# Kernel optimization log

Measured on AMD Instinct MI355X. Metric: run time of the kernel, lower is better.

## Reference

```python
import jax, jax.numpy as jnp
import numpy as np

D = 1024
H = 16
HD = D // H
FF = 4096
B = 2
S = 2048


def _layer_norm(x, g, b, eps=1e-5):
    mu = jnp.mean(x, axis=-1, keepdims=True)
    var = jnp.mean(jnp.square(x - mu), axis=-1, keepdims=True)
    return (x - mu) * jax.lax.rsqrt(var + eps) * g + b


def setup_inputs() -> dict:
    key = jax.random.key(0)
    ks = jax.random.split(key, 16)
    s = 0.02
    return {
        "x": jax.random.normal(ks[0], (B, S, D), jnp.float32),
        "Wq": jax.random.normal(ks[1], (H, D, HD), jnp.float32) * s,
        "bq": jnp.zeros((H, HD), jnp.float32),
        "Wk": jax.random.normal(ks[2], (H, D, HD), jnp.float32) * s,
        "bk": jnp.zeros((H, HD), jnp.float32),
        "Wv": jax.random.normal(ks[3], (H, D, HD), jnp.float32) * s,
        "bv": jnp.zeros((H, HD), jnp.float32),
        "Wo": jax.random.normal(ks[4], (D, D), jnp.float32) * s,
        "bo": jnp.zeros((D,), jnp.float32),
        "W1": jax.random.normal(ks[5], (D, FF), jnp.float32) * s,
        "b1": jnp.zeros((FF,), jnp.float32),
        "W2": jax.random.normal(ks[6], (FF, D), jnp.float32) * s,
        "b2": jnp.zeros((D,), jnp.float32),
        "g1": jnp.ones((D,), jnp.float32),
        "be1": jnp.zeros((D,), jnp.float32),
        "g2": jnp.ones((D,), jnp.float32),
        "be2": jnp.zeros((D,), jnp.float32),
    }


def reference(x, Wq, bq, Wk, bk, Wv, bv, Wo, bo, W1, b1, W2, b2, g1, be1, g2, be2):
    b, s, d = x.shape
    # per-head projections (vectorized over heads)
    q = jnp.einsum("bsd,hde->bhse", x, Wq) + bq[None, :, None, :]
    k = jnp.einsum("bsd,hde->bhse", x, Wk) + bk[None, :, None, :]
    v = jnp.einsum("bsd,hde->bhse", x, Wv) + bv[None, :, None, :]
    # NOTE: source scales by 1/dim_k (not 1/sqrt(dim_k)) -- kept faithful
    scores = jnp.einsum("bhse,bhte->bhst", q, k) / jnp.asarray(HD, x.dtype)
    causal = jnp.tril(jnp.ones((s, s), bool))  # [S,S]
    scores = jnp.where(causal[None, None], scores, jnp.asarray(-jnp.inf, x.dtype))
    attn = jax.nn.softmax(scores, axis=-1)
    ctx = jnp.einsum("bhst,bhte->bhse", attn, v)  # [B,H,S,hd]
    ctx = jnp.transpose(ctx, (0, 2, 1, 3)).reshape(b, s, d)  # concat heads
    attn_out = ctx @ Wo + bo
    x = _layer_norm(x + attn_out, g1, be1)
    # feed-forward: linear -> exact GELU -> linear (dropout = eval identity)
    h = jax.nn.gelu(x @ W1 + b1, approximate=False)
    ff = h @ W2 + b2
    return _layer_norm(x + ff, g2, be2)
```

## Files before the change

kernel.cpp:

```cpp
#include <hip/hip_runtime.h>
#include <math.h>

constexpr int Dm  = 1024;
constexpr int Hh  = 16;
constexpr int HDm = 64;
constexpr int FFm = 4096;
constexpr int Bb  = 2;
constexpr int Sq  = 2048;
constexpr int Mm  = Bb * Sq;

typedef __attribute__((ext_vector_type(8))) short short8;
typedef __attribute__((ext_vector_type(4))) short short4v;
typedef __attribute__((ext_vector_type(4))) float f32x4;

#define AS1 __attribute__((address_space(1)))
#define AS3 __attribute__((address_space(3)))

constexpr float QSCALE = 0.022542110013890054f;

__device__ __forceinline__ unsigned short f2b(float f) {
    union { float f; unsigned u; } v; v.f = f;
    unsigned r = v.u + 0x7FFFu + ((v.u >> 16) & 1u);
    return (unsigned short)(r >> 16);
}

__global__ __launch_bounds__(256) void convert_x(const float* __restrict__ x,
                                                 short* __restrict__ xb) {
    int i = blockIdx.x * 256 + threadIdx.x;
    float4 v = ((const float4*)x)[i];
    short4v o;
    o[0] = (short)f2b(v.x); o[1] = (short)f2b(v.y);
    o[2] = (short)f2b(v.z); o[3] = (short)f2b(v.w);
    ((short4v*)xb)[i] = o;
}

__global__ __launch_bounds__(256) void transpose_to_bf16(
    const float* __restrict__ src, short* __restrict__ dst, int R, int C) {
    __shared__ float t[64][65];
    const int c0 = blockIdx.x * 64, r0 = blockIdx.y * 64;
    const int lc = threadIdx.x & 63, lr4 = threadIdx.x >> 6;
    #pragma unroll
    for (int p = 0; p < 16; ++p) {
        int rr = p * 4 + lr4;
        t[rr][lc] = src[(size_t)(r0 + rr) * C + c0 + lc];
    }
    __syncthreads();
    #pragma unroll
    for (int p = 0; p < 16; ++p) {
        int rr = p * 4 + lr4;
        dst[(size_t)(c0 + rr) * R + r0 + lc] = (short)f2b(t[lc][rr]);
    }
}

__global__ __launch_bounds__(256) void build_wqkv(
    const float* __restrict__ Wq, const float* __restrict__ Wk,
    const float* __restrict__ Wv, short* __restrict__ dst) {
    const int kt = blockIdx.x, h = blockIdx.y, which = blockIdx.z;
    const float* W = ((which == 0) ? Wq : (which == 1) ? Wk : Wv) +
                     (size_t)h * Dm * HDm;
    __shared__ float t[64][65];
    const int lc = threadIdx.x & 63, lr4 = threadIdx.x >> 6;
    #pragma unroll
    for (int p = 0; p < 16; ++p) {
        int kr = p * 4 + lr4;
        t[kr][lc] = W[(size_t)(kt * 64 + kr) * HDm + lc];
    }
    __syncthreads();
    const int nbase = which * 1024 + h * 64;
    #pragma unroll
    for (int p = 0; p < 16; ++p) {
        int e = p * 4 + lr4;
        dst[(size_t)(nbase + e) * Dm + kt * 64 + lc] = (short)f2b(t[lc][e]);
    }
}

__global__ __launch_bounds__(256) void build_bqkv(
    const float* __restrict__ bq, const float* __restrict__ bk,
    const float* __restrict__ bv, float* __restrict__ bcat) {
    int n = blockIdx.x * 256 + threadIdx.x;
    const float* s = (n < 1024) ? bq : (n < 2048) ? bk : bv;
    bcat[n] = s[n & 1023];
}

template<int EPI>
__global__ __launch_bounds__(512, 2) void gemm256(
    const short* __restrict__ A, const short* __restrict__ Bt,
    const float* __restrict__ bias,
    short* __restrict__ outb,
    short* __restrict__ qo, short* __restrict__ ko, short* __restrict__ vo,
    int K, int N, int NMT)
{
    __shared__ __align__(16) char lds[131072];
    char* const ldsA = lds;
    char* const ldsB = lds + 65536;
    const int tid = threadIdx.x;
    const int l = tid & 63, wv = tid >> 6;
    const int wm = wv >> 2, wn = wv & 3;
    const int lr = l & 15, lg = l >> 4;
    const int bid = blockIdx.x;
    const int m0 = (bid % NMT) * 256;
    const int n0 = (bid / NMT) * 256;
    const size_t KB = (size_t)K * 2;
    const int NT = K >> 6;

    const char* pA[2][2];
    const char* pB[2][2];
    #pragma unroll
    for (int i = 0; i < 2; ++i) {
        int c = tid + 512 * i;
        int rh = c >> 3, j = c & 7;
        int sw = (j ^ (rh & 7)) << 4;
        #pragma unroll
        for (int h = 0; h < 2; ++h) {
            pA[h][i] = (const char*)A + (size_t)(m0 + h * 128 + rh) * KB + sw;
            pB[h][i] = (const char*)Bt + (size_t)(n0 + h * 128 + rh) * KB + sw;
        }
    }
    const int dbase = tid * 16;

    f32x4 acc[8][4];
    f32x4 z4 = {0.f, 0.f, 0.f, 0.f};
    #pragma unroll
    for (int i = 0; i < 8; ++i)
        #pragma unroll
        for (int j = 0; j < 4; ++j) acc[i][j] = z4;

#define STAGE_B(h, nb) do {                                                     \
    char* _b = ldsB + ((nb) * 2 + (h)) * 16384;                                 \
    __builtin_amdgcn_global_load_lds((const AS1 void*)pB[h][0],                 \
        (AS3 void*)(_b + dbase), 16, 0, 0);                                     \
    __builtin_amdgcn_global_load_lds((const AS1 void*)pB[h][1],                 \
        (AS3 void*)(_b + dbase + 8192), 16, 0, 0);                              \
    pB[h][0] += 128; pB[h][1] += 128; } while (0)
#define STAGE_A(h, nb) do {                                                     \
    char* _a = ldsA + ((nb) * 2 + (h)) * 16384;                                 \
    __builtin_amdgcn_global_load_lds((const AS1 void*)pA[h][0],                 \
        (AS3 void*)(_a + dbase), 16, 0, 0);                                     \
    __builtin_amdgcn_global_load_lds((const AS1 void*)pA[h][1],                 \
        (AS3 void*)(_a + dbase + 8192), 16, 0, 0);                              \
    pA[h][0] += 128; pA[h][1] += 128; } while (0)

    STAGE_B(0, 0); STAGE_B(1, 0); STAGE_A(0, 0); STAGE_A(1, 0);
    asm volatile("s_waitcnt vmcnt(2)" ::: "memory");
    __builtin_amdgcn_s_barrier();
    __builtin_amdgcn_sched_barrier(0);

    const int swk0 = ((0 + lg) ^ (lr & 7)) << 4;
    const int swk1 = ((4 + lg) ^ (lr & 7)) << 4;

    for (int kt = 0; kt < NT; ++kt) {
        const int buf = kt & 1, nbuf = buf ^ 1;
        const bool more = (kt + 1 < NT);
        char* const Ah0 = ldsA + (buf * 2) * 16384;
        char* const Ah1 = ldsA + (buf * 2 + 1) * 16384;
        char* const Bh  = ldsB + (buf * 2 + (wn >> 1)) * 16384 + (wn & 1) * 8192;

        short8 bf[4][2];
        #pragma unroll
        for (int nf = 0; nf < 4; ++nf) {
            const char* bb = Bh + (nf * 16 + lr) * 128;
            bf[nf][0] = *(const short8*)(bb + swk0);
            bf[nf][1] = *(const short8*)(bb + swk1);
        }
        short8 af[2][2];

#define LOAD_A(p) do {                                                          \
    _Pragma("unroll")                                                           \
    for (int j2 = 0; j2 < 2; ++j2) {                                            \
        const int mf = 2 * (p) + j2;                                            \
        const char* ab = ((mf >> 2) ? Ah1 : Ah0) +                              \
                         ((mf & 3) * 32 + wm * 16 + lr) * 128;                  \
        af[j2][0] = *(const short8*)(ab + swk0);                                \
        af[j2][1] = *(const short8*)(ab + swk1);                                \
    } } while (0)

#define MFMA8(p) do {                                                           \
    _Pragma("unroll")                                                           \
    for (int j2 = 0; j2 < 2; ++j2)                                              \
        _Pragma("unroll")                                                       \
        for (int nf = 0; nf < 4; ++nf) {                                        \
            acc[2 * (p) + j2][nf] = __builtin_amdgcn_mfma_f32_16x16x32_bf16(    \
                af[j2][0], bf[nf][0], acc[2 * (p) + j2][nf], 0, 0, 0);          \
            acc[2 * (p) + j2][nf] = __builtin_amdgcn_mfma_f32_16x16x32_bf16(    \
                af[j2][1], bf[nf][1], acc[2 * (p) + j2][nf], 0, 0, 0);          \
        } } while (0)

        LOAD_A(0);
        if (more) STAGE_B(0, nbuf);
        __builtin_amdgcn_s_barrier();
        asm volatile("s_waitcnt lgkmcnt(0)" ::: "memory");
        __builtin_amdgcn_sched_barrier(0);
        __builtin_amdgcn_s_setprio(1);
        MFMA8(0);
        __builtin_amdgcn_s_setprio(0);
        __builtin_amdgcn_s_barrier();
        LOAD_A(1);
        if (more) STAGE_B(1, nbuf);
        __builtin_amdgcn_s_barrier();
        asm volatile("s_waitcnt lgkmcnt(0)" ::: "memory");
        __builtin_amdgcn_sched_barrier(0);
        __builtin_amdgcn_s_setprio(1);
        MFMA8(1);
        __builtin_amdgcn_s_setprio(0);
        if (more) asm volatile("s_waitcnt vmcnt(4)" ::: "memory");
        else      asm volatile("s_waitcnt vmcnt(0)" ::: "memory");
        __builtin_amdgcn_s_barrier();
        __builtin_amdgcn_sched_barrier(0);
        LOAD_A(2);
        if (more) STAGE_A(0, nbuf);
        __builtin_amdgcn_s_barrier();
        asm volatile("s_waitcnt lgkmcnt(0)" ::: "memory");
        __builtin_amdgcn_sched_barrier(0);
        __builtin_amdgcn_s_setprio(1);
        MFMA8(2);
        __builtin_amdgcn_s_setprio(0);
        __builtin_amdgcn_s_barrier();
        LOAD_A(3);
        if (more) STAGE_A(1, nbuf);
        __builtin_amdgcn_s_barrier();
        asm volatile("s_waitcnt lgkmcnt(0)" ::: "memory");
        __builtin_amdgcn_sched_barrier(0);
        __builtin_amdgcn_s_setprio(1);
        MFMA8(3);
        __builtin_amdgcn_s_setprio(0);
        asm volatile("s_waitcnt vmcnt(2)" ::: "memory");
        __builtin_amdgcn_s_barrier();
        __builtin_amdgcn_sched_barrier(0);
#undef LOAD_A
#undef MFMA8
    }

    #pragma unroll
    for (int mf = 0; mf < 8; ++mf) {
        #pragma unroll
        for (int nf = 0; nf < 4; ++nf) {
            const int n = n0 + wn * 64 + nf * 16 + lr;
            const int mB = m0 + mf * 32 + wm * 16 + lg * 4;
            if (EPI == 1) {
                #pragma unroll
                for (int r = 0; r < 4; ++r) {
                    float val = acc[mf][nf][r] + bias[n];
                    val = 0.5f * val * (1.0f + erff(val * 0.70710678118654752f));
                    outb[(size_t)(mB + r) * N + n] = (short)f2b(val);
                }
            } else {
                const int which = n >> 10, hh = (n >> 6) & 15, e = n & 63;
                const int bb2 = mB >> 11, ss = mB & 2047;
                if (which == 2) {
                    short4v pk;
                    #pragma unroll
                    for (int r = 0; r < 4; ++r)
                        pk[r] = (short)f2b(acc[mf][nf][r] + bias[n]);
                    *(short4v*)&vo[(((size_t)bb2 * Hh + hh) * HDm + e) * Sq + ss] = pk;
                } else {
                    short* o = (which == 0) ? qo : ko;
                    const float sc = (which == 0) ? QSCALE : 1.0f;
                    #pragma unroll
                    for (int r = 0; r < 4; ++r) {
                        float val = (acc[mf][nf][r] + bias[n]) * sc;
                        o[(((size_t)bb2 * Hh + hh) * Sq + ss + r) * HDm + e] = (short)f2b(val);
                    }
                }
            }
        }
    }
#undef STAGE_A
#undef STAGE_B
}

template<int EPI, int BM>
__global__ __launch_bounds__(256) void gemm_bf16(
    const short* __restrict__ A, const short* __restrict__ Bt,
    const float* __restrict__ bias, const float* __restrict__ res,
    float* __restrict__ outf, short* __restrict__ outb,
    int K, int N)
{
    constexpr int BMW = BM / 2;
    constexpr int MF  = BMW / 16;
    __shared__ __align__(16) char smem[BM * 128 + 16384];
    char* ldsA = smem;
    char* ldsB = smem + BM * 128;
    const int tid = threadIdx.x;
    const int l = tid & 63, wv = tid >> 6;
    const int wr = wv >> 1, wc = wv & 1, lr = l & 15, lg = l >> 4;
    const int m0 = blockIdx.x * BM, n0 = blockIdx.y * 128;
    const size_t KB = (size_t)K * 2;
    const char* Ab = (const char*)A;
    const char* Bb = (const char*)Bt;

    f32x4 zero4 = {0.f, 0.f, 0.f, 0.f};
    f32x4 acc[MF][4];
    #pragma unroll
    for (int i = 0; i < MF; ++i)
        #pragma unroll
        for (int j = 0; j < 4; ++j) acc[i][j] = zero4;

    for (int k0 = 0; k0 < K; k0 += 64) {
        __syncthreads();
        #pragma unroll
        for (int r = 0; r < BM / 32; ++r) {
            int c  = (wv * (BM / 32) + r) * 64;
            int cl = c + l;
            int row = cl >> 3, j = cl & 7;
            int sw = ((j ^ (row & 7)) << 4);
            __builtin_amdgcn_global_load_lds(
                (const AS1 void*)(Ab + (size_t)(m0 + row) * KB + (size_t)k0 * 2 + sw),
                (AS3 void*)(ldsA + c * 16), 16, 0, 0);
        }
        #pragma unroll
        for (int r = 0; r < 4; ++r) {
            int c  = (wv * 4 + r) * 64;
            int cl = c + l;
            int row = cl >> 3, j = cl & 7;
            int sw = ((j ^ (row & 7)) << 4);
            __builtin_amdgcn_global_load_lds(
                (const AS1 void*)(Bb + (size_t)(n0 + row) * KB + (size_t)k0 * 2 + sw),
                (AS3 void*)(ldsB + c * 16), 16, 0, 0);
        }
        __syncthreads();
        #pragma unroll
        for (int ks = 0; ks < 2; ++ks) {
            short8 af[MF], bf[4];
            #pragma unroll
            for (int i = 0; i < MF; ++i) {
                int rowA = wr * BMW + i * 16 + lr;
                af[i] = *(const short8*)(ldsA + rowA * 128 +
                            (((ks * 4 + lg) ^ (rowA & 7)) << 4));
            }
            #pragma unroll
            for (int i = 0; i < 4; ++i) {
                int rowB = wc * 64 + i * 16 + lr;
                bf[i] = *(const short8*)(ldsB + rowB * 128 +
                            (((ks * 4 + lg) ^ (rowB & 7)) << 4));
            }
            #pragma unroll
            for (int i = 0; i < MF; ++i)
                #pragma unroll
                for (int jn = 0; jn < 4; ++jn)
                    acc[i][jn] = __builtin_amdgcn_mfma_f32_16x16x32_bf16(
                        af[i], bf[jn], acc[i][jn], 0, 0, 0);
        }
    }

    #pragma unroll
    for (int i = 0; i < MF; ++i) {
        #pragma unroll
        for (int jn = 0; jn < 4; ++jn) {
            #pragma unroll
            for (int r = 0; r < 4; ++r) {
                int m = m0 + wr * BMW + i * 16 + lg * 4 + r;
                int n = n0 + wc * 64 + jn * 16 + lr;
                float val = acc[i][jn][r];
                if (EPI == 0) {
                    val += bias[n] + res[(size_t)m * N + n];
                    outf[(size_t)m * N + n] = val;
                } else {
                    val += bias[n];
                    val = 0.5f * val * (1.0f + erff(val * 0.70710678118654752f));
                    outb[(size_t)m * N + n] = (short)f2b(val);
                }
            }
        }
    }
}

__global__ __launch_bounds__(256) void attn_mfma(
    const short* __restrict__ qg, const short* __restrict__ kg,
    const short* __restrict__ vtg, short* __restrict__ ctx)
{
    const int bid = blockIdx.x;
    const int qt = (Sq / 64 - 1) - (bid >> 5);
    const int hb = bid & 31;
    const int h = hb & 15, b = hb >> 4;
    const int tid = threadIdx.x;
    const int l = tid & 63, wv = tid >> 6;
    const int lr = l & 15, lg = l >> 4;

    __shared__ __align__(16) char KlB[8192];
    __shared__ __align__(16) char VtB[8192];
    __shared__ __align__(16) char PlB[4][2048];

    const size_t bh = ((size_t)b * Hh + h) * Sq;
    const size_t vbase = ((size_t)b * Hh + h) * HDm * Sq;

    const int qbase = qt * 64 + wv * 16;
    short8 aq[2];
    #pragma unroll
    for (int ks = 0; ks < 2; ++ks)
        aq[ks] = *(const short8*)(qg + (bh + qbase + lr) * HDm + ks * 32 + lg * 8);

    f32x4 zero4 = {0.f, 0.f, 0.f, 0.f};
    f32x4 oacc[4], lacc = zero4;
    #pragma unroll
    for (int i = 0; i < 4; ++i) oacc[i] = zero4;
    float mreg[4];
    #pragma unroll
    for (int r = 0; r < 4; ++r) mreg[r] = -3e38f;

    short8 vone;
    #pragma unroll
    for (int j = 0; j < 8; ++j) vone[j] = (short)0x3F80;

    char* plw = PlB[wv];

    const char* srcK[2]; const char* srcV[2];
    #pragma unroll
    for (int r2 = 0; r2 < 2; ++r2) {
        int cl = tid + 256 * r2;
        int row = cl >> 3, j = cl & 7;
        srcK[r2] = (const char*)kg + ((bh + row) * HDm + ((j ^ (row & 7)) * 8)) * 2;
        srcV[r2] = (const char*)vtg + (vbase + (size_t)row * Sq + ((j ^ (row & 7)) * 8)) * 2;
    }

    const int nt = qt + 1;
    for (int tk = 0; tk < nt; ++tk) {
        __syncthreads();
        #pragma unroll
        for (int r2 = 0; r2 < 2; ++r2) {
            int c = tid + 256 * r2;
            __builtin_amdgcn_global_load_lds((const AS1 void*)srcK[r2],
                (AS3 void*)(KlB + c * 16), 16, 0, 0);
            srcK[r2] += 64 * HDm * 2;
            __builtin_amdgcn_global_load_lds((const AS1 void*)srcV[r2],
                (AS3 void*)(VtB + c * 16), 16, 0, 0);
            srcV[r2] += 64 * 2;
        }
        __syncthreads();

        f32x4 sc[4];
        #pragma unroll
        for (int i = 0; i < 4; ++i) sc[i] = zero4;
        __builtin_amdgcn_s_setprio(1);
        #pragma unroll
        for (int kd = 0; kd < 2; ++kd) {
            #pragma unroll
            for (int nf = 0; nf < 4; ++nf) {
                short8 bk = *(const short8*)(KlB + (nf * 16 + lr) * 128 +
                                (((kd * 4 + lg) ^ (lr & 7)) << 4));
                sc[nf] = __builtin_amdgcn_mfma_f32_16x16x32_bf16(
                    aq[kd], bk, sc[nf], 0, 0, 0);
            }
        }
        __builtin_amdgcn_s_setprio(0);

        if (tk == qt) {
            #pragma unroll
            for (int r = 0; r < 4; ++r) {
                const int qglob = qbase + lg * 4 + r;
                #pragma unroll
                for (int nf = 0; nf < 4; ++nf)
                    if (tk * 64 + nf * 16 + lr > qglob) sc[nf][r] = -3e38f;
            }
        }

        float lm[4];
        #pragma unroll
        for (int r = 0; r < 4; ++r)
            lm[r] = fmaxf(fmaxf(sc[0][r], sc[1][r]), fmaxf(sc[2][r], sc[3][r]));
        bool grow = (lm[0] > mreg[0] + 8.f) || (lm[1] > mreg[1] + 8.f) ||
                    (lm[2] > mreg[2] + 8.f) || (lm[3] > mreg[3] + 8.f);

        if (__any((int)grow)) {
            #pragma unroll
            for (int r = 0; r < 4; ++r) {
                float mr = lm[r];
                #pragma unroll
                for (int o = 1; o < 16; o <<= 1)
                    mr = fmaxf(mr, __shfl_xor(mr, o));
                float mnew = fmaxf(mreg[r], mr);
                float cf = exp2f(mreg[r] - mnew);
                mreg[r] = mnew;
                const int prow = lg * 4 + r;
                #pragma unroll
                for (int nf = 0; nf < 4; ++nf) {
                    float p = exp2f(sc[nf][r] - mnew);
                    *(unsigned short*)(plw + prow * 128 +
                        (((nf * 2 + (lr >> 3)) ^ (prow & 7)) << 4) +
                        ((lr & 7) << 1)) = (unsigned short)(__float_as_uint(p) >> 16);
                }
                #pragma unroll
                for (int nf = 0; nf < 4; ++nf) oacc[nf][r] *= cf;
                lacc[r] *= cf;
            }
        } else {
            #pragma unroll
            for (int r = 0; r < 4; ++r) {
                const int prow = lg * 4 + r;
                #pragma unroll
                for (int nf = 0; nf < 4; ++nf) {
                    float p = exp2f(sc[nf][r] - mreg[r]);
                    *(unsigned short*)(plw + prow * 128 +
                        (((nf * 2 + (lr >> 3)) ^ (prow & 7)) << 4) +
                        ((lr & 7) << 1)) = (unsigned short)(__float_as_uint(p) >> 16);
                }
            }
        }

        asm volatile("s_waitcnt lgkmcnt(0)" ::: "memory");
        __builtin_amdgcn_sched_barrier(0);

        __builtin_amdgcn_s_setprio(1);
        #pragma unroll
        for (int ks = 0; ks < 2; ++ks) {
            short8 pa = *(const short8*)(plw + lr * 128 +
                            (((ks * 4 + lg) ^ (lr & 7)) << 4));
            #pragma unroll
            for (int nf = 0; nf < 4; ++nf) {
                short8 bv8 = *(const short8*)(VtB + (nf * 16 + lr) * 128 +
                                (((ks * 4 + lg) ^ (lr & 7)) << 4));
                oacc[nf] = __builtin_amdgcn_mfma_f32_16x16x32_bf16(
                    pa, bv8, oacc[nf], 0, 0, 0);
            }
            lacc = __builtin_amdgcn_mfma_f32_16x16x32_bf16(pa, vone, lacc, 0, 0, 0);
        }
        __builtin_amdgcn_s_setprio(0);
    }

    #pragma unroll
    for (int r = 0; r < 4; ++r) {
        float inv = 1.0f / lacc[r];
        int q = qbase + lg * 4 + r;
        size_t o = ((size_t)b * Sq + q) * Dm + h * HDm;
        #pragma unroll
        for (int nf = 0; nf < 4; ++nf)
            ctx[o + nf * 16 + lr] = (short)f2b(oacc[nf][r] * inv);
    }
}

template<int BF16OUT>
__global__ __launch_bounds__(256) void ln_kernel(
    const float* __restrict__ in, const float* __restrict__ g,
    const float* __restrict__ be, float* __restrict__ outf,
    short* __restrict__ outb)
{
    const int m = blockIdx.x;
    const int tid = threadIdx.x;
    const float4 vl = *(const float4*)&in[(size_t)m * Dm + tid * 4];
    float s  = vl.x + vl.y + vl.z + vl.w;
    float s2 = vl.x * vl.x + vl.y * vl.y + vl.z * vl.z + vl.w * vl.w;
    #pragma unroll
    for (int o = 32; o > 0; o >>= 1) {
        s  += __shfl_down(s, o);
        s2 += __shfl_down(s2, o);
    }
    __shared__ float rs[4], rs2[4];
    const int w = tid >> 6;
    if ((tid & 63) == 0) { rs[w] = s; rs2[w] = s2; }
    __syncthreads();
    s  = rs[0] + rs[1] + rs[2] + rs[3];
    s2 = rs2[0] + rs2[1] + rs2[2] + rs2[3];
    const float mean = s * (1.0f / Dm);
    const float var  = s2 * (1.0f / Dm) - mean * mean;
    const float rstd = rsqrtf(var + 1e-5f);
    const float4 gv = *(const float4*)&g[tid * 4];
    const float4 bv = *(const float4*)&be[tid * 4];
    float4 ov;
    ov.x = (vl.x - mean) * rstd * gv.x + bv.x;
    ov.y = (vl.y - mean) * rstd * gv.y + bv.y;
    ov.z = (vl.z - mean) * rstd * gv.z + bv.z;
    ov.w = (vl.w - mean) * rstd * gv.w + bv.w;
    *(float4*)&outf[(size_t)m * Dm + tid * 4] = ov;
    if (BF16OUT) {
        short4v o4;
        o4[0] = (short)f2b(ov.x); o4[1] = (short)f2b(ov.y);
        o4[2] = (short)f2b(ov.z); o4[3] = (short)f2b(ov.w);
        *(short4v*)&outb[(size_t)m * Dm + tid * 4] = o4;
    }
}

extern "C" void kernel_launch(void* const* d_in, const int* in_sizes, int n_in,
                              void* d_out, int out_size, void* d_ws, size_t ws_size,
                              hipStream_t stream)
{
    const float* x  = (const float*)d_in[0];
    const float* Wq = (const float*)d_in[1];
    const float* bq = (const float*)d_in[2];
    const float* Wk = (const float*)d_in[3];
    const float* bk = (const float*)d_in[4];
    const float* Wv = (const float*)d_in[5];
    const float* bv = (const float*)d_in[6];
    const float* Wo = (const float*)d_in[7];
    const float* bo = (const float*)d_in[8];
    const float* W1 = (const float*)d_in[9];
    const float* b1 = (const float*)d_in[10];
    const float* W2 = (const float*)d_in[11];
    const float* b2 = (const float*)d_in[12];
    const float* g1 = (const float*)d_in[13];
    const float* be1= (const float*)d_in[14];
    const float* g2 = (const float*)d_in[15];
    const float* be2= (const float*)d_in[16];
    float* out = (float*)d_out;

    char* ws = (char*)d_ws;
    size_t off = 0;
    auto alloc = [&](size_t bytes) {
        char* p = ws + off;
        off += (bytes + 255) & ~(size_t)255;
        return p;
    };
    const size_t MD2 = (size_t)Mm * Dm * 2;
    short* xb    = (short*)alloc(MD2);
    short* wqkvt = (short*)alloc((size_t)3072 * Dm * 2);
    float* bcat  = (float*)alloc(3072 * 4);
    short* wot   = (short*)alloc((size_t)Dm * Dm * 2);
    short* w1t   = (short*)alloc((size_t)FFm * Dm * 2);
    short* w2t   = (short*)alloc((size_t)Dm * FFm * 2);
    short* qb    = (short*)alloc(MD2);
    short* kb    = (short*)alloc(MD2);
    short* vtb   = (short*)alloc(MD2);
    short* ctxb  = (short*)alloc(MD2);
    short* hb    = qb;
    float* y     = (float*)alloc((size_t)Mm * Dm * 4);
    float* x1f   = (float*)alloc((size_t)Mm * Dm * 4);
    short* x1b   = (short*)alloc(MD2);
    float* y2    = y;

    convert_x<<<Mm * Dm / 1024, 256, 0, stream>>>(x, xb);
    build_wqkv<<<dim3(16, 16, 3), 256, 0, stream>>>(Wq, Wk, Wv, wqkvt);
    build_bqkv<<<12, 256, 0, stream>>>(bq, bk, bv, bcat);
    transpose_to_bf16<<<dim3(16, 16), 256, 0, stream>>>(Wo, wot, Dm, Dm);
    transpose_to_bf16<<<dim3(64, 16), 256, 0, stream>>>(W1, w1t, Dm, FFm);
    transpose_to_bf16<<<dim3(16, 64), 256, 0, stream>>>(W2, w2t, FFm, Dm);

    gemm256<2><<<192, 512, 0, stream>>>(
        xb, wqkvt, bcat, nullptr, qb, kb, vtb, Dm, 3072, 16);
    attn_mfma<<<1024, 256, 0, stream>>>(qb, kb, vtb, ctxb);
    gemm_bf16<0, 64><<<dim3(64, 8), 256, 0, stream>>>(
        ctxb, wot, bo, x, y, nullptr, Dm, Dm);
    ln_kernel<1><<<Mm, 256, 0, stream>>>(y, g1, be1, x1f, x1b);
    gemm256<1><<<256, 512, 0, stream>>>(
        x1b, w1t, b1, hb, nullptr, nullptr, nullptr, Dm, FFm, 16);
    gemm_bf16<0, 64><<<dim3(64, 8), 256, 0, stream>>>(
        hb, w2t, b2, x1f, y2, nullptr, FFm, Dm);
    ln_kernel<0><<<Mm, 256, 0, stream>>>(y2, g2, be2, out, nullptr);
}
```

Measured before the change: 255.6 us.

## Replace output-projection GEMMs with double-buffered 128x128 pipelined MFMA kernel

Replaces the single-buffered 64x128-tile bf16 GEMM used for the Wo and W2 projections with a 128x128-tile kernel. The new kernel double-buffers A and B tiles in 64 KB of LDS and splits each k-step into two MFMA halves. The next tile's async global-to-LDS loads are issued between the halves, with explicit vmcnt waits, barriers and setprio, so memory traffic overlaps with MFMA work. The larger tile halves the grid to 256 blocks, which improves data reuse per block but reduces the number of blocks available to hide latency. The kernel also keeps a leftover redundant LDS load line.

```diff
diff --git a/kernel.cpp b/kernel.cpp
--- a/kernel.cpp
+++ b/kernel.cpp
@@ -268,89 +268,155 @@
 #undef STAGE_B
 }
 
-template<int EPI, int BM>
-__global__ __launch_bounds__(256) void gemm_bf16(
+template<int EPI>
+__global__ __launch_bounds__(256, 2) void gemm128dp(
     const short* __restrict__ A, const short* __restrict__ Bt,
     const float* __restrict__ bias, const float* __restrict__ res,
     float* __restrict__ outf, short* __restrict__ outb,
     int K, int N)
 {
-    constexpr int BMW = BM / 2;
-    constexpr int MF  = BMW / 16;
-    __shared__ __align__(16) char smem[BM * 128 + 16384];
-    char* ldsA = smem;
-    char* ldsB = smem + BM * 128;
+    __shared__ __align__(16) char lds[65536];
+    char* const ldsA = lds;
+    char* const ldsB = lds + 32768;
     const int tid = threadIdx.x;
     const int l = tid & 63, wv = tid >> 6;
-    const int wr = wv >> 1, wc = wv & 1, lr = l & 15, lg = l >> 4;
-    const int m0 = blockIdx.x * BM, n0 = blockIdx.y * 128;
+    const int wr = wv >> 1, wc = wv & 1;
+    const int lr = l & 15, lg = l >> 4;
+    const int m0 = blockIdx.x * 128, n0 = blockIdx.y * 128;
     const size_t KB = (size_t)K * 2;
-    const char* Ab = (const char*)A;
-    const char* Bb = (const char*)Bt;
-
-    f32x4 zero4 = {0.f, 0.f, 0.f, 0.f};
-    f32x4 acc[MF][4];
-    #pragma unroll
-    for (int i = 0; i < MF; ++i)
-        #pragma unroll
-        for (int j = 0; j < 4; ++j) acc[i][j] = zero4;
-
-    for (int k0 = 0; k0 < K; k0 += 64) {
-        __syncthreads();
-        #pragma unroll
-        for (int r = 0; r < BM / 32; ++r) {
-            int c  = (wv * (BM / 32) + r) * 64;
-            int cl = c + l;
-            int row = cl >> 3, j = cl & 7;
-            int sw = ((j ^ (row & 7)) << 4);
-            __builtin_amdgcn_global_load_lds(
-                (const AS1 void*)(Ab + (size_t)(m0 + row) * KB + (size_t)k0 * 2 + sw),
-                (AS3 void*)(ldsA + c * 16), 16, 0, 0);
-        }
-        #pragma unroll
-        for (int r = 0; r < 4; ++r) {
-            int c  = (wv * 4 + r) * 64;
-            int cl = c + l;
-            int row = cl >> 3, j = cl & 7;
-            int sw = ((j ^ (row & 7)) << 4);
-            __builtin_amdgcn_global_load_lds(
-                (const AS1 void*)(Bb + (size_t)(n0 + row) * KB + (size_t)k0 * 2 + sw),
-                (AS3 void*)(ldsB + c * 16), 16, 0, 0);
-        }
-        __syncthreads();
-        #pragma unroll
-        for (int ks = 0; ks < 2; ++ks) {
-            short8 af[MF], bf[4];
+    const int NT = K >> 6;
+
+    const int r0 = tid >> 3, jj = tid & 7;
+    const int sw = (jj ^ (r0 & 7)) << 4;
+    const char* aSrc[4]; const char* bSrc1[2]; const char* bSrc2[2];
+    #pragma unroll
+    for (int i = 0; i < 4; ++i)
+        aSrc[i] = (const char*)A + (size_t)(m0 + r0 + 32 * i) * KB + sw;
+    #pragma unroll
+    for (int i = 0; i < 2; ++i) {
+        bSrc1[i] = (const char*)Bt + (size_t)(n0 + r0 + 64 * i) * KB + sw;
+        bSrc2[i] = (const char*)Bt + (size_t)(n0 + 32 + r0 + 64 * i) * KB + sw;
+    }
+    const int aDst0 = tid * 16;
+
+#define STAGE_SA(nb) do {                                                       \
+    char* _a = ldsA + (nb) * 16384;                                             \
+    _Pragma("unroll")                                                           \
+    for (int i = 0; i < 4; ++i) {                                               \
+        __builtin_amdgcn_global_load_lds((const AS1 void*)aSrc[i],              \
+            (AS3 void*)(_a + aDst0 + i * 4096), 16, 0, 0);                      \
+        aSrc[i] += 128;                                                         \
+    } } while (0)
+#define STAGE_SB1(nb) do {                                                      \
+    char* _b = ldsB + (nb) * 16384;                                             \
+    _Pragma("unroll")                                                           \
+    for (int i = 0; i < 2; ++i) {                                               \
+        __builtin_amdgcn_global_load_lds((const AS1 void*)bSrc1[i],             \
+            (AS3 void*)(_b + aDst0 + i * 8192), 16, 0, 0);                      \
+        bSrc1[i] += 128;                                                        \
+    } } while (0)
+#define STAGE_SB2(nb) do {                                                      \
+    char* _b = ldsB + (nb) * 16384 + 4096;                                      \
+    _Pragma("unroll")                                                           \
+    for (int i = 0; i < 2; ++i) {                                               \
+        __builtin_amdgcn_global_load_lds((const AS1 void*)bSrc2[i],             \
+            (AS3 void*)(_b + aDst0 + i * 8192), 16, 0, 0);                      \
+        bSrc2[i] += 128;                                                        \
+    } } while (0)
+
+    f32x4 acc[4][4];
+    f32x4 z4 = {0.f, 0.f, 0.f, 0.f};
+    #pragma unroll
+    for (int i = 0; i < 4; ++i)
+        #pragma unroll
+        for (int j = 0; j < 4; ++j) acc[i][j] = z4;
+
+    STAGE_SA(0); STAGE_SB1(0); STAGE_SB2(0);
+    asm volatile("s_waitcnt vmcnt(2)" ::: "memory");
+    __builtin_amdgcn_s_barrier();
+    __builtin_amdgcn_sched_barrier(0);
+
+    const int swk0 = ((0 + lg) ^ (lr & 7)) << 4;
+    const int swk1 = ((4 + lg) ^ (lr & 7)) << 4;
+
+    for (int kt = 0; kt < NT; ++kt) {
+        const int buf = kt & 1, nbuf = buf ^ 1;
+        const bool more = (kt + 1 < NT);
+        char* const Ab = ldsA + buf * 16384;
+        char* const Bb = ldsB + buf * 16384;
+
+        short8 af[4][2], bf[2][2];
+        #pragma unroll
+        for (int mf = 0; mf < 4; ++mf) {
+            const int row = wr * 64 + mf * 16 + lr;
+            const char* ab = Ab + row * 128;
+            af[mf][0] = *(const short8*)(ab + ((0 + lg) ^ (row & 7) ? 0 : 0, swk0));
+            af[mf][0] = *(const short8*)(ab + (((0 + lg) ^ (row & 7)) << 4));
+            af[mf][1] = *(const short8*)(ab + (((4 + lg) ^ (row & 7)) << 4));
+        }
+        #pragma unroll
+        for (int nf = 0; nf < 2; ++nf) {
+            const int row = wc * 64 + nf * 16 + lr;
+            const char* bb = Bb + row * 128;
+            bf[nf][0] = *(const short8*)(bb + (((0 + lg) ^ (row & 7)) << 4));
+            bf[nf][1] = *(const short8*)(bb + (((4 + lg) ^ (row & 7)) << 4));
+        }
+        if (more) STAGE_SA(nbuf);
+        asm volatile("s_waitcnt lgkmcnt(0)" ::: "memory");
+        __builtin_amdgcn_sched_barrier(0);
+        __builtin_amdgcn_s_setprio(1);
+        #pragma unroll
+        for (int mf = 0; mf < 4; ++mf)
             #pragma unroll
-            for (int i = 0; i < MF; ++i) {
-                int rowA = wr * BMW + i * 16 + lr;
-                af[i] = *(const short8*)(ldsA + rowA * 128 +
-                            (((ks * 4 + lg) ^ (rowA & 7)) << 4));
-            }
+            for (int nf = 0; nf < 2; ++nf) {
+                acc[mf][nf] = __builtin_amdgcn_mfma_f32_16x16x32_bf16(
+                    af[mf][0], bf[nf][0], acc[mf][nf], 0, 0, 0);
+                acc[mf][nf] = __builtin_amdgcn_mfma_f32_16x16x32_bf16(
+                    af[mf][1], bf[nf][1], acc[mf][nf], 0, 0, 0);
+            }
+        __builtin_amdgcn_s_setprio(0);
+        if (more) asm volatile("s_waitcnt vmcnt(4)" ::: "memory");
+        else      asm volatile("s_waitcnt vmcnt(0)" ::: "memory");
+        __builtin_amdgcn_s_barrier();
+        __builtin_amdgcn_sched_barrier(0);
+
+        #pragma unroll
+        for (int nf = 0; nf < 2; ++nf) {
+            const int row = wc * 64 + (nf + 2) * 16 + lr;
+            const char* bb = Bb + row * 128;
+            bf[nf][0] = *(const short8*)(bb + (((0 + lg) ^ (row & 7)) << 4));
+            bf[nf][1] = *(const short8*)(bb + (((4 + lg) ^ (row & 7)) << 4));
+        }
+        if (more) { STAGE_SB1(nbuf); STAGE_SB2(nbuf); }
+        asm volatile("s_waitcnt lgkmcnt(0)" ::: "memory");
+        __builtin_amdgcn_sched_barrier(0);
+        __builtin_amdgcn_s_setprio(1);
+        #pragma unroll
+        for (int mf = 0; mf < 4; ++mf)
             #pragma unroll
-            for (int i = 0; i < 4; ++i) {
-                int rowB = wc * 64 + i * 16 + lr;
-                bf[i] = *(const short8*)(ldsB + rowB * 128 +
-                            (((ks * 4 + lg) ^ (rowB & 7)) << 4));
-            }
-            #pragma unroll
-            for (int i = 0; i < MF; ++i)
-                #pragma unroll
-                for (int jn = 0; jn < 4; ++jn)
-                    acc[i][jn] = __builtin_amdgcn_mfma_f32_16x16x32_bf16(
-                        af[i], bf[jn], acc[i][jn], 0, 0, 0);
-        }
-    }
-
-    #pragma unroll
-    for (int i = 0; i < MF; ++i) {
-        #pragma unroll
-        for (int jn = 0; jn < 4; ++jn) {
+            for (int nf = 0; nf < 2; ++nf) {
+                acc[mf][nf + 2] = __builtin_amdgcn_mfma_f32_16x16x32_bf16(
+                    af[mf][0], bf[nf][0], acc[mf][nf + 2], 0, 0, 0);
+                acc[mf][nf + 2] = __builtin_amdgcn_mfma_f32_16x16x32_bf16(
+                    af[mf][1], bf[nf][1], acc[mf][nf + 2], 0, 0, 0);
+            }
+        __builtin_amdgcn_s_setprio(0);
+        if (more) {
+            asm volatile("s_waitcnt vmcnt(2)" ::: "memory");
+            __builtin_amdgcn_s_barrier();
+            __builtin_amdgcn_sched_barrier(0);
+        }
+    }
+
+    #pragma unroll
+    for (int mf = 0; mf < 4; ++mf) {
+        #pragma unroll
+        for (int nf = 0; nf < 4; ++nf) {
             #pragma unroll
             for (int r = 0; r < 4; ++r) {
-                int m = m0 + wr * BMW + i * 16 + lg * 4 + r;
-                int n = n0 + wc * 64 + jn * 16 + lr;
-                float val = acc[i][jn][r];
+                int m = m0 + wr * 64 + mf * 16 + lg * 4 + r;
+                int n = n0 + wc * 64 + nf * 16 + lr;
+                float val = acc[mf][nf][r];
                 if (EPI == 0) {
                     val += bias[n] + res[(size_t)m * N + n];
                     outf[(size_t)m * N + n] = val;
@@ -362,6 +428,9 @@
             }
         }
     }
+#undef STAGE_SA
+#undef STAGE_SB1
+#undef STAGE_SB2
 }
 
 __global__ __launch_bounds__(256) void attn_mfma(
@@ -625,12 +694,12 @@
     gemm256<2><<<192, 512, 0, stream>>>(
         xb, wqkvt, bcat, nullptr, qb, kb, vtb, Dm, 3072, 16);
     attn_mfma<<<1024, 256, 0, stream>>>(qb, kb, vtb, ctxb);
-    gemm_bf16<0, 64><<<dim3(64, 8), 256, 0, stream>>>(
+    gemm128dp<0><<<dim3(32, 8), 256, 0, stream>>>(
         ctxb, wot, bo, x, y, nullptr, Dm, Dm);
     ln_kernel<1><<<Mm, 256, 0, stream>>>(y, g1, be1, x1f, x1b);
     gemm256<1><<<256, 512, 0, stream>>>(
         x1b, w1t, b1, hb, nullptr, nullptr, nullptr, Dm, FFm, 16);
-    gemm_bf16<0, 64><<<dim3(64, 8), 256, 0, stream>>>(
+    gemm128dp<0><<<dim3(32, 8), 256, 0, stream>>>(
         hb, w2t, b2, x1f, y2, nullptr, FFm, Dm);
     ln_kernel<0><<<Mm, 256, 0, stream>>>(y2, g2, be2, out, nullptr);
 }
```

Result: no change. 252.7 us (-1.1%).
